# Kernel optimization log

Hardware: AMD Instinct MI355X
Metric: run time of the kernel (lower is better)

The kernel has to match this reference:

```python
import jax, jax.numpy as jnp
import numpy as np

BS, D, C, L_MAP, N_LAYERS, IMG = 8, 512, 128, 8, 9, 64


def _leaky(x):
    return jnp.where(x >= 0, x, 0.2 * x)


def _conv2d_mod(x, style, weight):
    # x: [bs, C, H, W], style: [bs, C], weight: [Cout, Cin, 3, 3]
    # modulate along input-channel dim, demodulate per (sample, out-channel)
    mw = weight[None] * style[:, None, :, None, None]          # [bs, Cout, Cin, 3, 3]
    rstd = jax.lax.rsqrt(jnp.sum(mw * mw, axis=(2, 3, 4), keepdims=True) + 1e-8)
    dw = mw * rstd                                             # demodulated per-sample weights

    def per_sample(xi, wi):
        return jax.lax.conv_general_dilated(
            xi[None], wi, window_strides=(1, 1), padding='SAME',
            dimension_numbers=('NCHW', 'OIHW', 'NCHW'))[0]

    return jax.vmap(per_sample)(x, dw)                         # [bs, C, H, W]


def _upsample2x(x):
    b, c, h, w = x.shape
    return jax.image.resize(x, (b, c, 2 * h, 2 * w), method='bilinear')


def setup_inputs():
    key = jax.random.key(0)
    ks = jax.random.split(key, 10)
    # kaiming fan_in gain for leaky_relu(a=0) per nn.init in Conv2dMod
    conv_std = float(np.sqrt(2.0 / (C * 9)))
    return {
        'latent_z': jax.random.normal(ks[0], (BS, D), jnp.float32),
        'noise': jax.random.normal(ks[1], (N_LAYERS, BS, IMG * IMG), jnp.float32),
        'map_w': jax.random.normal(ks[2], (L_MAP, D, D), jnp.float32) / np.sqrt(D),
        'map_b': jnp.zeros((L_MAP, D), jnp.float32),
        'A_w': jax.random.normal(ks[3], (N_LAYERS, D, C), jnp.float32) / np.sqrt(D),
        'A_b': jax.random.normal(ks[4], (N_LAYERS, C), jnp.float32) * 0.02 + 1.0,
        'B_w': jax.random.normal(ks[5], (N_LAYERS, C), jnp.float32),
        'B_b': jax.random.normal(ks[6], (N_LAYERS, C), jnp.float32) * 0.02,
        'conv_w': jax.random.normal(ks[7], (N_LAYERS, C, C, 3, 3), jnp.float32) * conv_std,
        'rgb_w': jax.random.normal(ks[8], (3, C, 3, 3), jnp.float32) / np.sqrt(C * 9),
        'rgb_b': jnp.zeros((3,), jnp.float32),
    }


def reference(latent_z, noise, map_w, map_b, A_w, A_b, B_w, B_b, conv_w, rgb_w, rgb_b):
    # ---- Mapping: PixelNorm + n_map_layers FC+LeakyReLU ----
    w = latent_z * jax.lax.rsqrt(jnp.mean(latent_z * latent_z, axis=1, keepdims=True) + 1e-8)
    for i in range(L_MAP):
        w = _leaky(w @ map_w[i] + map_b[i])                    # [bs, D] (same w for every style layer)

    # ---- Synthesis ----
    x = jnp.zeros((BS, C, 4, 4), latent_z.dtype)
    for i in range(N_LAYERS):
        if i % 2 == 1:
            x = _upsample2x(x)
        b, c, h, wd = x.shape
        ns = h * wd
        style = w @ A_w[i] + A_b[i]                            # [bs, C]
        # B: Linear(1, C) on per-pixel noise scalar -> per-channel noise map
        nmap = noise[i][:, :ns, None] * B_w[i][None, None, :] + B_b[i]  # [bs, ns, C]
        nmap = jnp.transpose(nmap, (0, 2, 1)).reshape(b, C, h, wd)
        x = _leaky(_conv2d_mod(x, style, conv_w[i]) + nmap)

    # ---- to RGB ----
    rgb = jax.lax.conv_general_dilated(
        x, rgb_w, window_strides=(1, 1), padding='SAME',
        dimension_numbers=('NCHW', 'OIHW', 'NCHW')) + rgb_b[None, :, None, None]
    return rgb
```

## Files before the change

### kernel.cpp

```cpp
#include <hip/hip_runtime.h>
#include <hip/hip_bf16.h>

#define BS 8
#define D 512
#define CCH 128
#define LMAP 8
#define NLAYERS 9

typedef short short8 __attribute__((ext_vector_type(8)));
typedef short short4v __attribute__((ext_vector_type(4)));
typedef float f32x4 __attribute__((ext_vector_type(4)));

__device__ short g_bufA[(size_t)BS * 4096 * CCH];
__device__ short g_bufB[(size_t)BS * 4096 * CCH];
__device__ float g_w[2][BS * D];
__device__ float g_style_all[NLAYERS * BS * CCH];
__device__ float g_rstd_all[NLAYERS * BS * CCH];
__device__ float g_s2[(size_t)NLAYERS * CCH * CCH];
__device__ short g_wpack[(size_t)NLAYERS * 9 * 4 * 8 * 64 * 8];
__device__ short g_rgbpack[9 * 4 * 64 * 8];

__device__ __forceinline__ float leaky(float v) { return v >= 0.f ? v : 0.2f * v; }
__device__ __forceinline__ short f2b(float f) {
    __hip_bfloat16 h = __float2bfloat16(f);
    return *reinterpret_cast<short*>(&h);
}
__device__ __forceinline__ float b2f(short s) {
    return __uint_as_float(((unsigned int)(unsigned short)s) << 16);
}
__device__ __forceinline__ int swz(int col) { return ((col ^ (col >> 3)) & 7) << 3; }

__device__ __forceinline__ void uptaps(int o, int Win, int& i0, int& i1, float& w0, float& w1)
{
    int m = o >> 1;
    if ((o & 1) == 0) { i0 = m - 1; i1 = m; w0 = 0.25f; w1 = 0.75f; if (i0 < 0) { i0 = 0; w0 = 0.f; w1 = 1.f; } }
    else              { i0 = m; i1 = m + 1; w0 = 0.75f; w1 = 0.25f; if (i1 >= Win) { i1 = Win - 1; w0 = 1.f; w1 = 0.f; } }
}

#define WPN (NLAYERS * 9 * 4 * 8 * 64)
#define RGBN (9 * 4 * 64)
#define S2N (NLAYERS * CCH * CCH)
#define NPREPB ((WPN + RGBN + S2N + 255) / 256)
#define NMAPB (32 * BS)

__global__ __launch_bounds__(256) void prep_map0_kernel(
    const float* __restrict__ z, const float* __restrict__ W0, const float* __restrict__ b0,
    const float* __restrict__ convw, const float* __restrict__ rgbw)
{
    const int bid = blockIdx.x;
    const int tid = threadIdx.x;
    if (bid < NMAPB) {
        const int jt = bid & 31, b = bid >> 5;
        const int jb = jt * 16;
        const int jl = tid & 15, kp = tid >> 4;
        __shared__ float xin[D];
        __shared__ float part[16][16];
        __shared__ float wred[4];
        xin[tid] = z[b * D + tid];
        xin[tid + 256] = z[b * D + tid + 256];
        __syncthreads();
        {
            float p = xin[tid] * xin[tid] + xin[tid + 256] * xin[tid + 256];
#pragma unroll
            for (int off = 32; off > 0; off >>= 1) p += __shfl_down(p, off, 64);
            if ((tid & 63) == 0) wred[tid >> 6] = p;
            __syncthreads();
            float ss = wred[0] + wred[1] + wred[2] + wred[3];
            float r = rsqrtf(ss * (1.f / 512.f) + 1e-8f);
            xin[tid] *= r; xin[tid + 256] *= r;
            __syncthreads();
        }
        const float* Wp = W0 + jb + jl;
        const int k0 = kp * 32;
        float a[16];
#pragma unroll
        for (int j = 0; j < 16; ++j) a[j] = 0.f;
#pragma unroll
        for (int k = k0; k < k0 + 32; k += 16) {
#pragma unroll
            for (int j = 0; j < 16; ++j)
                a[j] += xin[k + j] * Wp[(size_t)(k + j) * D];
        }
        float s16 = 0.f;
#pragma unroll
        for (int j = 0; j < 16; ++j) s16 += a[j];
        part[kp][jl] = s16;
        __syncthreads();
        if (tid < 16) {
            float s = b0[jb + tid];
#pragma unroll
            for (int p = 0; p < 16; ++p) s += part[p][tid];
            g_w[1][b * D + jb + tid] = leaky(s);
        }
        return;
    }
    int idx = (bid - NMAPB) * 256 + tid;
    if (idx < WPN) {
        int lane = idx & 63;
        int cogrp = (idx >> 6) & 7;
        int chunk = (idx >> 9) & 3;
        int t = idx >> 11;
        int layer = t / 9, tap = t - layer * 9;
        int co = cogrp * 16 + (lane & 15);
        int ci0 = chunk * 32 + (lane >> 4) * 8;
        short8 v;
#pragma unroll
        for (int j = 0; j < 8; ++j)
            v[j] = f2b(convw[(((size_t)layer * CCH + co) * CCH + ci0 + j) * 9 + tap]);
        *reinterpret_cast<short8*>(&g_wpack[(size_t)idx * 8]) = v;
    } else if (idx < WPN + RGBN) {
        int u = idx - WPN;
        int lane = u & 63;
        int chunk = (u >> 6) & 3;
        int tap = u >> 8;
        int co = lane & 15;
        int ci0 = chunk * 32 + (lane >> 4) * 8;
        short8 v;
#pragma unroll
        for (int j = 0; j < 8; ++j)
            v[j] = (co < 3) ? f2b(rgbw[((size_t)(co * CCH) + ci0 + j) * 9 + tap]) : (short)0;
        *reinterpret_cast<short8*>(&g_rgbpack[(size_t)u * 8]) = v;
    } else if (idx < WPN + RGBN + S2N) {
        int u = idx - WPN - RGBN;
        const float* wp = convw + (size_t)u * 9;
        float s = 0.f;
#pragma unroll
        for (int t = 0; t < 9; ++t) { float m = wp[t]; s += m * m; }
        g_s2[u] = s;
    }
}

__global__ __launch_bounds__(256) void map_fc_kernel(
    int srcSel, const float* __restrict__ W, const float* __restrict__ bias)
{
    float* wout = g_w[srcSel ^ 1];
    int b = blockIdx.y;
    int jb = blockIdx.x * 16;
    int tid = threadIdx.x;
    int jl = tid & 15, kp = tid >> 4;
    __shared__ float xin[D];
    __shared__ float part[16][16];
    const float* win = g_w[srcSel];
    xin[tid] = win[b * D + tid];
    xin[tid + 256] = win[b * D + tid + 256];
    __syncthreads();
    const float* Wp = W + jb + jl;
    const int k0 = kp * 32;
    float a[16];
#pragma unroll
    for (int j = 0; j < 16; ++j) a[j] = 0.f;
#pragma unroll
    for (int k = k0; k < k0 + 32; k += 16) {
#pragma unroll
        for (int j = 0; j < 16; ++j)
            a[j] += xin[k + j] * Wp[(size_t)(k + j) * D];
    }
    float s16 = 0.f;
#pragma unroll
    for (int j = 0; j < 16; ++j) s16 += a[j];
    part[kp][jl] = s16;
    __syncthreads();
    if (tid < 16) {
        float s = bias[jb + tid];
#pragma unroll
        for (int p = 0; p < 16; ++p) s += part[p][tid];
        wout[b * D + jb + tid] = leaky(s);
    }
}

__global__ __launch_bounds__(256) void style_rstd_kernel(
    const float* __restrict__ Aw, const float* __restrict__ Ab)
{
    int l = blockIdx.x + 1;
    int b = blockIdx.y;
    int tid = threadIdx.x;
    __shared__ float ws_[D];
    __shared__ float part[2][CCH];
    __shared__ float st[CCH];
    ws_[tid] = g_w[0][b * D + tid];
    ws_[tid + 256] = g_w[0][b * D + tid + 256];
    __syncthreads();
    {
        int c = tid & 127, kh = tid >> 7;
        const float* Ap = Aw + (size_t)l * D * CCH + c;
        const int k0 = kh * 256;
        float a0 = 0.f, a1 = 0.f, a2 = 0.f, a3 = 0.f, a4 = 0.f, a5 = 0.f, a6 = 0.f, a7 = 0.f;
        for (int k = k0; k < k0 + 256; k += 8) {
            a0 += ws_[k + 0] * Ap[(size_t)(k + 0) * CCH];
            a1 += ws_[k + 1] * Ap[(size_t)(k + 1) * CCH];
            a2 += ws_[k + 2] * Ap[(size_t)(k + 2) * CCH];
            a3 += ws_[k + 3] * Ap[(size_t)(k + 3) * CCH];
            a4 += ws_[k + 4] * Ap[(size_t)(k + 4) * CCH];
            a5 += ws_[k + 5] * Ap[(size_t)(k + 5) * CCH];
            a6 += ws_[k + 6] * Ap[(size_t)(k + 6) * CCH];
            a7 += ws_[k + 7] * Ap[(size_t)(k + 7) * CCH];
        }
        part[kh][c] = ((a0 + a1) + (a2 + a3)) + ((a4 + a5) + (a6 + a7));
    }
    __syncthreads();
    if (tid < CCH) {
        float s = part[0][tid] + part[1][tid] + Ab[l * CCH + tid];
        st[tid] = s;
        g_style_all[((size_t)l * BS + b) * CCH + tid] = s;
    }
    __syncthreads();
    int colid = tid >> 4, kpart = tid & 15;
#pragma unroll
    for (int co8 = 0; co8 < 8; ++co8) {
        int cout = co8 * 16 + colid;
        const float* sp = g_s2 + ((size_t)l * CCH + cout) * CCH + kpart * 8;
        float s = 0.f;
#pragma unroll
        for (int j = 0; j < 8; ++j) { float sv = st[kpart * 8 + j]; s += sv * sv * sp[j]; }
#pragma unroll
        for (int off = 8; off > 0; off >>= 1) s += __shfl_down(s, off, 16);
        if (kpart == 0) g_rstd_all[((size_t)l * BS + b) * CCH + cout] = rsqrtf(s + 1e-8f);
    }
}

__global__ __launch_bounds__(256) void conv8_pair_kernel(
    const float* __restrict__ noise,
    const float* __restrict__ Bw, const float* __restrict__ Bb)
{
    constexpr int W = 8, SW = 10, ROWS = 10, NS = 64, WIN = 4;
    const int b = blockIdx.x;
    const int tid = threadIdx.x;
    const int lane = tid & 63;
    const int wave = tid >> 6;
    const int wpx = wave & 1;
    const int wco = wave >> 1;

    __shared__ short xs1[ROWS * SW * CCH];
    __shared__ short xs2[ROWS * SW * CCH];
    __shared__ short sm[16 * CCH];
    __shared__ float style2_s[CCH], style3_s[CCH];

    if (tid < CCH) {
        style2_s[tid] = g_style_all[((size_t)2 * BS + b) * CCH + tid];
        style3_s[tid] = g_style_all[((size_t)3 * BS + b) * CCH + tid];
    }
    for (int u = tid; u < 16 * CCH; u += 256) {
        int c = u & 127;
        int pp = u >> 7;
        float v = leaky(noise[b * 4096 + pp] * Bw[c] + Bb[c])
                  * g_style_all[((size_t)1 * BS + b) * CCH + c];
        sm[u] = f2b(v);
    }
    for (int u = tid; u < ROWS * SW * 16; u += 256) {
        int ck = u & 15;
        int cell = u >> 4;
        int col = cell % SW;
        int rr = cell / SW;
        if (rr >= 1 && rr <= 8 && col >= 1 && col <= 8) continue;
        short8 zz = {0, 0, 0, 0, 0, 0, 0, 0};
        *reinterpret_cast<short8*>(&xs2[(((rr * SW + col) * CCH) + ck * 8) ^ swz(col)]) = zz;
    }
    __syncthreads();

    for (int u = tid; u < ROWS * SW * 16; u += 256) {
        int ck = u & 15;
        int rem = u >> 4;
        int col = rem % SW;
        int rr = rem / SW;
        int gy = rr - 1, gx = col - 1;
        short8 v = {0, 0, 0, 0, 0, 0, 0, 0};
        if (gy >= 0 && gy < W && gx >= 0 && gx < W) {
            int y0, y1, x0, x1; float wy0, wy1, wx0, wx1;
            uptaps(gy, WIN, y0, y1, wy0, wy1);
            uptaps(gx, WIN, x0, x1, wx0, wx1);
            short8 a00 = *reinterpret_cast<const short8*>(&sm[((size_t)y0 * WIN + x0) * CCH + ck * 8]);
            short8 a01 = *reinterpret_cast<const short8*>(&sm[((size_t)y0 * WIN + x1) * CCH + ck * 8]);
            short8 a10 = *reinterpret_cast<const short8*>(&sm[((size_t)y1 * WIN + x0) * CCH + ck * 8]);
            short8 a11 = *reinterpret_cast<const short8*>(&sm[((size_t)y1 * WIN + x1) * CCH + ck * 8]);
            float w00 = wy0 * wx0, w01 = wy0 * wx1, w10 = wy1 * wx0, w11 = wy1 * wx1;
#pragma unroll
            for (int j = 0; j < 8; ++j)
                v[j] = f2b(w00 * b2f(a00[j]) + w01 * b2f(a01[j])
                         + w10 * b2f(a10[j]) + w11 * b2f(a11[j]));
        }
        *reinterpret_cast<short8*>(&xs1[(((rr * SW + col) * CCH) + ck * 8) ^ swz(col)]) = v;
    }
    __syncthreads();

    int rL[2], cL[2];
#pragma unroll
    for (int pf = 0; pf < 2; ++pf) {
        int pl = (wpx * 2 + pf) * 16 + (lane & 15);
        cL[pf] = pl & (W - 1);
        rL[pf] = pl >> 3;
    }
    const int grpoff = (lane >> 4) * 8;

    {
        f32x4 acc[2][4] = {};
        const short* wl = g_wpack + ((size_t)1 * 9 * 4 * 8 * 64 + (size_t)(wco * 4) * 64 + lane) * 8;
        short8 wc0 = *reinterpret_cast<const short8*>(wl);
        short8 wc1 = *reinterpret_cast<const short8*>(wl + 512);
        short8 wc2 = *reinterpret_cast<const short8*>(wl + 1024);
        short8 wc3 = *reinterpret_cast<const short8*>(wl + 1536);
#pragma unroll
        for (int k = 0; k < 36; ++k) {
            short8 wn0 = wc0, wn1 = wc1, wn2 = wc2, wn3 = wc3;
            if (k + 1 < 36) {
                const short* wk = wl + (size_t)(k + 1) * 4096;
                wn0 = *reinterpret_cast<const short8*>(wk);
                wn1 = *reinterpret_cast<const short8*>(wk + 512);
                wn2 = *reinterpret_cast<const short8*>(wk + 1024);
                wn3 = *reinterpret_cast<const short8*>(wk + 1536);
            }
            const int tap = k >> 2, ch = k & 3;
            const int ky = tap / 3, kx = tap - ky * 3;
#pragma unroll
            for (int pf = 0; pf < 2; ++pf) {
                int col = cL[pf] + kx;
                int idx = (((rL[pf] + ky) * SW + col) * CCH + (ch << 5) + grpoff) ^ swz(col);
                short8 xf = *reinterpret_cast<const short8*>(&xs1[idx]);
                acc[pf][0] = __builtin_amdgcn_mfma_f32_16x16x32_bf16(wc0, xf, acc[pf][0], 0, 0, 0);
                acc[pf][1] = __builtin_amdgcn_mfma_f32_16x16x32_bf16(wc1, xf, acc[pf][1], 0, 0, 0);
                acc[pf][2] = __builtin_amdgcn_mfma_f32_16x16x32_bf16(wc2, xf, acc[pf][2], 0, 0, 0);
                acc[pf][3] = __builtin_amdgcn_mfma_f32_16x16x32_bf16(wc3, xf, acc[pf][3], 0, 0, 0);
            }
            wc0 = wn0; wc1 = wn1; wc2 = wn2; wc3 = wn3;
        }
        float nz[2];
#pragma unroll
        for (int pf = 0; pf < 2; ++pf)
            nz[pf] = noise[(size_t)BS * 4096 + b * 4096 + (wpx * 2 + pf) * 16 + (lane & 15)];
#pragma unroll
        for (int cf = 0; cf < 4; ++cf) {
            const int coB = (wco * 4 + cf) * 16 + (lane >> 4) * 4;
            float rs[4], bw[4], bb[4], sn[4];
#pragma unroll
            for (int r = 0; r < 4; ++r) {
                rs[r] = g_rstd_all[((size_t)1 * BS + b) * CCH + coB + r];
                bw[r] = Bw[1 * CCH + coB + r];
                bb[r] = Bb[1 * CCH + coB + r];
                sn[r] = style2_s[coB + r];
            }
#pragma unroll
            for (int pf = 0; pf < 2; ++pf) {
                int px = (wpx * 2 + pf) * 16 + (lane & 15);
                int y = px >> 3, x = px & 7;
                short4v o;
#pragma unroll
                for (int r = 0; r < 4; ++r)
                    o[r] = f2b(leaky(acc[pf][cf][r] * rs[r] + nz[pf] * bw[r] + bb[r]) * sn[r]);
                int col = x + 1;
                *reinterpret_cast<short4v*>(&xs2[((((y + 1) * SW + col) * CCH) + coB) ^ swz(col)]) = o;
            }
        }
    }
    __syncthreads();

    {
        f32x4 acc[2][4] = {};
        const short* wl = g_wpack + ((size_t)2 * 9 * 4 * 8 * 64 + (size_t)(wco * 4) * 64 + lane) * 8;
        short8 wc0 = *reinterpret_cast<const short8*>(wl);
        short8 wc1 = *reinterpret_cast<const short8*>(wl + 512);
        short8 wc2 = *reinterpret_cast<const short8*>(wl + 1024);
        short8 wc3 = *reinterpret_cast<const short8*>(wl + 1536);
#pragma unroll
        for (int k = 0; k < 36; ++k) {
            short8 wn0 = wc0, wn1 = wc1, wn2 = wc2, wn3 = wc3;
            if (k + 1 < 36) {
                const short* wk = wl + (size_t)(k + 1) * 4096;
                wn0 = *reinterpret_cast<const short8*>(wk);
                wn1 = *reinterpret_cast<const short8*>(wk + 512);
                wn2 = *reinterpret_cast<const short8*>(wk + 1024);
                wn3 = *reinterpret_cast<const short8*>(wk + 1536);
            }
            const int tap = k >> 2, ch = k & 3;
            const int ky = tap / 3, kx = tap - ky * 3;
#pragma unroll
            for (int pf = 0; pf < 2; ++pf) {
                int col = cL[pf] + kx;
                int idx = (((rL[pf] + ky) * SW + col) * CCH + (ch << 5) + grpoff) ^ swz(col);
                short8 xf = *reinterpret_cast<const short8*>(&xs2[idx]);
                acc[pf][0] = __builtin_amdgcn_mfma_f32_16x16x32_bf16(wc0, xf, acc[pf][0], 0, 0, 0);
                acc[pf][1] = __builtin_amdgcn_mfma_f32_16x16x32_bf16(wc1, xf, acc[pf][1], 0, 0, 0);
                acc[pf][2] = __builtin_amdgcn_mfma_f32_16x16x32_bf16(wc2, xf, acc[pf][2], 0, 0, 0);
                acc[pf][3] = __builtin_amdgcn_mfma_f32_16x16x32_bf16(wc3, xf, acc[pf][3], 0, 0, 0);
            }
            wc0 = wn0; wc1 = wn1; wc2 = wn2; wc3 = wn3;
        }
        float nz[2];
#pragma unroll
        for (int pf = 0; pf < 2; ++pf)
            nz[pf] = noise[(size_t)2 * BS * 4096 + b * 4096 + (wpx * 2 + pf) * 16 + (lane & 15)];
#pragma unroll
        for (int cf = 0; cf < 4; ++cf) {
            const int coB = (wco * 4 + cf) * 16 + (lane >> 4) * 4;
            float rs[4], bw[4], bb[4], sn[4];
#pragma unroll
            for (int r = 0; r < 4; ++r) {
                rs[r] = g_rstd_all[((size_t)2 * BS + b) * CCH + coB + r];
                bw[r] = Bw[2 * CCH + coB + r];
                bb[r] = Bb[2 * CCH + coB + r];
                sn[r] = style3_s[coB + r];
            }
#pragma unroll
            for (int pf = 0; pf < 2; ++pf) {
                int px = (wpx * 2 + pf) * 16 + (lane & 15);
                short4v o;
#pragma unroll
                for (int r = 0; r < 4; ++r)
                    o[r] = f2b(leaky(acc[pf][cf][r] * rs[r] + nz[pf] * bw[r] + bb[r]) * sn[r]);
                *reinterpret_cast<short4v*>(&g_bufA[((size_t)b * NS + px) * CCH + coB]) = o;
            }
        }
    }
}

template<int LW, int UPM, int TLW>
__global__ __launch_bounds__(256) void conv_mfma_kernel(
    int srcSel, int layer, int layerNext,
    const float* __restrict__ noise,
    const float* __restrict__ Bw, const float* __restrict__ Bb)
{
    constexpr int W = 1 << LW;
    constexpr int TW = 1 << TLW;
    constexpr int TH = 64 >> TLW;
    constexpr int SW = TW + 2;
    constexpr int ROWS = TH + 2;
    constexpr int NS = W * W;
    constexpr int WIN = W / 2;
    constexpr int TILES_X = W / TW;

    const short* xin = srcSel ? g_bufB : g_bufA;
    short* xout = srcSel ? g_bufA : g_bufB;

    const int b = blockIdx.x & 7;
    const int tileid = blockIdx.x >> 3;
    const int tx = tileid & (TILES_X - 1);
    const int ty = tileid >> (LW - TLW);
    const int rowBase = ty * TH;
    const int colBase = tx * TW;
    const int tid = threadIdx.x;
    const int lane = tid & 63;
    const int wave = tid >> 6;
    const int wpx = wave & 1;
    const int wco = wave >> 1;

    __shared__ short xs[ROWS * SW * CCH];
    __shared__ float style_s[CCH];

    if (tid < CCH)
        style_s[tid] = layerNext ? g_style_all[((size_t)layerNext * BS + b) * CCH + tid] : 1.f;

    {
        const short* src = xin + (size_t)b * NS * CCH;
        const short* srcH = xin + (size_t)b * WIN * WIN * CCH;
        constexpr int UN = ROWS * SW * 16;
        for (int u = tid; u < UN; u += 256) {
            int ck = u & 15;
            int rem = u >> 4;
            int col = rem % SW;
            int rr = rem / SW;
            int gy = rowBase + rr - 1, gx = colBase + col - 1;
            short8 v = {0, 0, 0, 0, 0, 0, 0, 0};
            if (gy >= 0 && gy < W && gx >= 0 && gx < W) {
                if (UPM == 0) {
                    v = *reinterpret_cast<const short8*>(&src[((size_t)gy * W + gx) * CCH + ck * 8]);
                } else {
                    int y0, y1, x0, x1; float wy0, wy1, wx0, wx1;
                    uptaps(gy, WIN, y0, y1, wy0, wy1);
                    uptaps(gx, WIN, x0, x1, wx0, wx1);
                    short8 a00 = *reinterpret_cast<const short8*>(&srcH[((size_t)y0 * WIN + x0) * CCH + ck * 8]);
                    short8 a01 = *reinterpret_cast<const short8*>(&srcH[((size_t)y0 * WIN + x1) * CCH + ck * 8]);
                    short8 a10 = *reinterpret_cast<const short8*>(&srcH[((size_t)y1 * WIN + x0) * CCH + ck * 8]);
                    short8 a11 = *reinterpret_cast<const short8*>(&srcH[((size_t)y1 * WIN + x1) * CCH + ck * 8]);
                    float w00 = wy0 * wx0, w01 = wy0 * wx1, w10 = wy1 * wx0, w11 = wy1 * wx1;
#pragma unroll
                    for (int j = 0; j < 8; ++j)
                        v[j] = f2b(w00 * b2f(a00[j]) + w01 * b2f(a01[j])
                                 + w10 * b2f(a10[j]) + w11 * b2f(a11[j]));
                }
            }
            *reinterpret_cast<short8*>(&xs[(((rr * SW + col) * CCH) + ck * 8) ^ swz(col)]) = v;
        }
    }
    __syncthreads();

    int rL[2], cL[2];
#pragma unroll
    for (int pf = 0; pf < 2; ++pf) {
        int pl = (wpx * 2 + pf) * 16 + (lane & 15);
        cL[pf] = pl & (TW - 1);
        rL[pf] = pl >> TLW;
    }
    const int grpoff = (lane >> 4) * 8;

    f32x4 acc[2][4] = {};
    const short* wl = g_wpack + ((size_t)layer * 9 * 4 * 8 * 64
                                 + (size_t)(wco * 4) * 64 + lane) * 8;

    short8 wc0 = *reinterpret_cast<const short8*>(wl);
    short8 wc1 = *reinterpret_cast<const short8*>(wl + 512);
    short8 wc2 = *reinterpret_cast<const short8*>(wl + 1024);
    short8 wc3 = *reinterpret_cast<const short8*>(wl + 1536);
#pragma unroll
    for (int k = 0; k < 36; ++k) {
        short8 wn0 = wc0, wn1 = wc1, wn2 = wc2, wn3 = wc3;
        if (k + 1 < 36) {
            const short* wk = wl + (size_t)(k + 1) * 4096;
            wn0 = *reinterpret_cast<const short8*>(wk);
            wn1 = *reinterpret_cast<const short8*>(wk + 512);
            wn2 = *reinterpret_cast<const short8*>(wk + 1024);
            wn3 = *reinterpret_cast<const short8*>(wk + 1536);
        }
        const int tap = k >> 2, ch = k & 3;
        const int ky = tap / 3, kx = tap - ky * 3;
#pragma unroll
        for (int pf = 0; pf < 2; ++pf) {
            int col = cL[pf] + kx;
            int idx = (((rL[pf] + ky) * SW + col) * CCH + (ch << 5) + grpoff) ^ swz(col);
            short8 xf = *reinterpret_cast<const short8*>(&xs[idx]);
            acc[pf][0] = __builtin_amdgcn_mfma_f32_16x16x32_bf16(wc0, xf, acc[pf][0], 0, 0, 0);
            acc[pf][1] = __builtin_amdgcn_mfma_f32_16x16x32_bf16(wc1, xf, acc[pf][1], 0, 0, 0);
            acc[pf][2] = __builtin_amdgcn_mfma_f32_16x16x32_bf16(wc2, xf, acc[pf][2], 0, 0, 0);
            acc[pf][3] = __builtin_amdgcn_mfma_f32_16x16x32_bf16(wc3, xf, acc[pf][3], 0, 0, 0);
        }
        wc0 = wn0; wc1 = wn1; wc2 = wn2; wc3 = wn3;
    }

    float nz[2];
    int pxg[2];
#pragma unroll
    for (int pf = 0; pf < 2; ++pf) {
        int pl = (wpx * 2 + pf) * 16 + (lane & 15);
        int x = pl & (TW - 1), y = pl >> TLW;
        pxg[pf] = (rowBase + y) * W + colBase + x;
        nz[pf] = noise[b * 4096 + pxg[pf]];
    }
#pragma unroll
    for (int cf = 0; cf < 4; ++cf) {
        const int coB = (wco * 4 + cf) * 16 + (lane >> 4) * 4;
        float rs[4], bw[4], bb[4], sn[4];
#pragma unroll
        for (int r = 0; r < 4; ++r) {
            rs[r] = g_rstd_all[((size_t)layer * BS + b) * CCH + coB + r];
            bw[r] = Bw[coB + r];
            bb[r] = Bb[coB + r];
            sn[r] = style_s[coB + r];
        }
#pragma unroll
        for (int pf = 0; pf < 2; ++pf) {
            short4v o;
#pragma unroll
            for (int r = 0; r < 4; ++r) {
                float v = leaky(acc[pf][cf][r] * rs[r] + nz[pf] * bw[r] + bb[r]) * sn[r];
                o[r] = f2b(v);
            }
            *reinterpret_cast<short4v*>(&xout[((size_t)b * NS + pxg[pf]) * CCH + coB]) = o;
        }
    }
}

__global__ __launch_bounds__(256) void rgb_mfma_kernel(
    int srcSel, const float* __restrict__ rgbb, float* __restrict__ out)
{
    constexpr int W = 64, TW = 32, TH = 2, SW = 34, ROWS = 4, NS = 4096;
    const short* xin = srcSel ? g_bufB : g_bufA;

    const int b = blockIdx.x & 7;
    const int tileid = blockIdx.x >> 3;
    const int tx = tileid & 1;
    const int ty = tileid >> 1;
    const int rowBase = ty * TH;
    const int colBase = tx * TW;
    const int tid = threadIdx.x;
    const int lane = tid & 63;
    const int wave = tid >> 6;

    __shared__ short xs[ROWS * SW * CCH];

    {
        const short* src = xin + (size_t)b * NS * CCH;
        constexpr int UN = ROWS * SW * 16;
        for (int u = tid; u < UN; u += 256) {
            int ck = u & 15;
            int rem = u >> 4;
            int col = rem % SW;
            int rr = rem / SW;
            int gy = rowBase + rr - 1, gx = colBase + col - 1;
            short8 v = {0, 0, 0, 0, 0, 0, 0, 0};
            if (gy >= 0 && gy < W && gx >= 0 && gx < W)
                v = *reinterpret_cast<const short8*>(&src[((size_t)gy * W + gx) * CCH + ck * 8]);
            *reinterpret_cast<short8*>(&xs[(((rr * SW + col) * CCH) + ck * 8) ^ swz(col)]) = v;
        }
    }
    __syncthreads();

    const int grpoff = (lane >> 4) * 8;
    const int cl = lane & 15;
    f32x4 acc[4] = {};
#pragma unroll
    for (int tap = 0; tap < 9; ++tap) {
        const int ky = tap / 3, kx = tap - ky * 3;
        short8 wf = *reinterpret_cast<const short8*>(
            &g_rgbpack[((size_t)(tap * 4 + wave) * 64 + lane) * 8]);
#pragma unroll
        for (int pf = 0; pf < 4; ++pf) {
            int pl = pf * 16 + cl;
            int x = pl & (TW - 1), y = pl >> 5;
            int col = x + kx;
            int idx = (((y + ky) * SW + col) * CCH + (wave << 5) + grpoff) ^ swz(col);
            short8 xf = *reinterpret_cast<const short8*>(&xs[idx]);
            acc[pf] = __builtin_amdgcn_mfma_f32_16x16x32_bf16(wf, xf, acc[pf], 0, 0, 0);
        }
    }
    __syncthreads();
    float* red = reinterpret_cast<float*>(xs);
    if (wave > 0) {
#pragma unroll
        for (int pf = 0; pf < 4; ++pf)
#pragma unroll
            for (int r = 0; r < 4; ++r)
                red[(((wave - 1) * 4 + pf) * 64 + lane) * 4 + r] = acc[pf][r];
    }
    __syncthreads();
    if (wave == 0 && (lane >> 4) == 0) {
#pragma unroll
        for (int pf = 0; pf < 4; ++pf) {
            int pl = pf * 16 + cl;
            int x = pl & (TW - 1), y = pl >> 5;
            int px = (rowBase + y) * W + colBase + x;
#pragma unroll
            for (int r = 0; r < 3; ++r) {
                float s = acc[pf][r];
#pragma unroll
                for (int wv = 0; wv < 3; ++wv)
                    s += red[((wv * 4 + pf) * 64 + lane) * 4 + r];
                out[(size_t)(b * 3 + r) * NS + px] = s + rgbb[r];
            }
        }
    }
}

extern "C" void kernel_launch(void* const* d_in, const int* in_sizes, int n_in,
                              void* d_out, int out_size, void* d_ws, size_t ws_size,
                              hipStream_t stream)
{
    const float* latent = (const float*)d_in[0];
    const float* noise  = (const float*)d_in[1];
    const float* map_w  = (const float*)d_in[2];
    const float* map_b  = (const float*)d_in[3];
    const float* A_w    = (const float*)d_in[4];
    const float* A_b    = (const float*)d_in[5];
    const float* B_w    = (const float*)d_in[6];
    const float* B_b    = (const float*)d_in[7];
    const float* conv_w = (const float*)d_in[8];
    const float* rgb_w  = (const float*)d_in[9];
    const float* rgb_b  = (const float*)d_in[10];
    float* out = (float*)d_out;
    (void)d_ws; (void)ws_size;

    prep_map0_kernel<<<NMAPB + NPREPB, 256, 0, stream>>>(latent, map_w, map_b, conv_w, rgb_w);

    int wsel = 1;
    for (int i = 1; i < LMAP; ++i) {
        map_fc_kernel<<<dim3(32, BS), 256, 0, stream>>>(
            wsel, map_w + (size_t)i * D * D, map_b + i * D);
        wsel ^= 1;
    }

    style_rstd_kernel<<<dim3(8, BS), 256, 0, stream>>>(A_w, A_b);

    conv8_pair_kernel<<<BS, 256, 0, stream>>>(noise, B_w, B_b);

    int cur = 0;
    int Hc = 8;
    for (int i = 3; i < NLAYERS; ++i) {
        if (i & 1) Hc *= 2;
        int ns = Hc * Hc;
        int lnext = (i < 8) ? (i + 1) : 0;
        int nblk = (ns / 64) * BS;
        const float* nz = noise + (size_t)i * BS * 4096;
        switch (i) {
            case 3: conv_mfma_kernel<4, 1, 4><<<nblk, 256, 0, stream>>>(cur, i, lnext, nz, B_w + i * CCH, B_b + i * CCH); break;
            case 4: conv_mfma_kernel<4, 0, 4><<<nblk, 256, 0, stream>>>(cur, i, lnext, nz, B_w + i * CCH, B_b + i * CCH); break;
            case 5: conv_mfma_kernel<5, 1, 5><<<nblk, 256, 0, stream>>>(cur, i, lnext, nz, B_w + i * CCH, B_b + i * CCH); break;
            case 6: conv_mfma_kernel<5, 0, 5><<<nblk, 256, 0, stream>>>(cur, i, lnext, nz, B_w + i * CCH, B_b + i * CCH); break;
            case 7: conv_mfma_kernel<6, 1, 5><<<nblk, 256, 0, stream>>>(cur, i, lnext, nz, B_w + i * CCH, B_b + i * CCH); break;
            case 8: conv_mfma_kernel<6, 0, 5><<<nblk, 256, 0, stream>>>(cur, i, lnext, nz, B_w + i * CCH, B_b + i * CCH); break;
        }
        cur ^= 1;
    }

    rgb_mfma_kernel<<<64 * BS, 256, 0, stream>>>(cur, rgb_b, out);
}
```

Before: 190.1 us.

## Fuse 16x16 conv layers 3 and 4 into one per-sample kernel

Adds a conv16_pair_kernel that upsamples the 8x8 activation into shared memory, runs layer 3's modulated conv, writes its result back into the same shared tile, then runs layer 4, all in one block per sample. This replaces two conv_mfma_kernel launches and the global round trip of the intermediate activation. In exchange, only BS=8 blocks run, so most CUs sit idle during these layers, and each wave does a long serial MFMA loop. The main loop now starts at layer 5 and switches buffer indices, which must line up with what the fused kernel writes.

New measurement: 234.8 us. +23.5%, slower.

```diff
diff --git a/kernel.cpp b/kernel.cpp
--- a/kernel.cpp
+++ b/kernel.cpp
@@ -401,6 +401,184 @@
 #pragma unroll
             for (int pf = 0; pf < 2; ++pf) {
                 int px = (wpx * 2 + pf) * 16 + (lane & 15);
+                short4v o;
+#pragma unroll
+                for (int r = 0; r < 4; ++r)
+                    o[r] = f2b(leaky(acc[pf][cf][r] * rs[r] + nz[pf] * bw[r] + bb[r]) * sn[r]);
+                *reinterpret_cast<short4v*>(&g_bufA[((size_t)b * NS + px) * CCH + coB]) = o;
+            }
+        }
+    }
+}
+
+__global__ __launch_bounds__(256) void conv16_pair_kernel(
+    const float* __restrict__ noise,
+    const float* __restrict__ Bw, const float* __restrict__ Bb)
+{
+    constexpr int W = 16, SW = 18, ROWS = 18, NS = 256, WIN = 8;
+    const int b = blockIdx.x;
+    const int tid = threadIdx.x;
+    const int lane = tid & 63;
+    const int wave = tid >> 6;
+    const int wpx = wave & 1;
+    const int wco = wave >> 1;
+
+    __shared__ short xs[ROWS * SW * CCH];
+    __shared__ float style4_s[CCH], style5_s[CCH];
+
+    if (tid < CCH) {
+        style4_s[tid] = g_style_all[((size_t)4 * BS + b) * CCH + tid];
+        style5_s[tid] = g_style_all[((size_t)5 * BS + b) * CCH + tid];
+    }
+
+    {
+        const short* src = g_bufA + (size_t)b * WIN * WIN * CCH;
+        for (int u = tid; u < ROWS * SW * 16; u += 256) {
+            int ck = u & 15;
+            int rem = u >> 4;
+            int col = rem % SW;
+            int rr = rem / SW;
+            int gy = rr - 1, gx = col - 1;
+            short8 v = {0, 0, 0, 0, 0, 0, 0, 0};
+            if (gy >= 0 && gy < W && gx >= 0 && gx < W) {
+                int y0, y1, x0, x1; float wy0, wy1, wx0, wx1;
+                uptaps(gy, WIN, y0, y1, wy0, wy1);
+                uptaps(gx, WIN, x0, x1, wx0, wx1);
+                short8 a00 = *reinterpret_cast<const short8*>(&src[((size_t)y0 * WIN + x0) * CCH + ck * 8]);
+                short8 a01 = *reinterpret_cast<const short8*>(&src[((size_t)y0 * WIN + x1) * CCH + ck * 8]);
+                short8 a10 = *reinterpret_cast<const short8*>(&src[((size_t)y1 * WIN + x0) * CCH + ck * 8]);
+                short8 a11 = *reinterpret_cast<const short8*>(&src[((size_t)y1 * WIN + x1) * CCH + ck * 8]);
+                float w00 = wy0 * wx0, w01 = wy0 * wx1, w10 = wy1 * wx0, w11 = wy1 * wx1;
+#pragma unroll
+                for (int j = 0; j < 8; ++j)
+                    v[j] = f2b(w00 * b2f(a00[j]) + w01 * b2f(a01[j])
+                             + w10 * b2f(a10[j]) + w11 * b2f(a11[j]));
+            }
+            *reinterpret_cast<short8*>(&xs[(((rr * SW + col) * CCH) + ck * 8) ^ swz(col)]) = v;
+        }
+    }
+    __syncthreads();
+
+    int rL[8], cL[8];
+#pragma unroll
+    for (int pf = 0; pf < 8; ++pf) {
+        int pl = wpx * 128 + pf * 16 + (lane & 15);
+        cL[pf] = pl & (W - 1);
+        rL[pf] = pl >> 4;
+    }
+    const int grpoff = (lane >> 4) * 8;
+
+    {
+        f32x4 acc[8][4] = {};
+        const short* wl = g_wpack + ((size_t)3 * 9 * 4 * 8 * 64 + (size_t)(wco * 4) * 64 + lane) * 8;
+        short8 wc0 = *reinterpret_cast<const short8*>(wl);
+        short8 wc1 = *reinterpret_cast<const short8*>(wl + 512);
+        short8 wc2 = *reinterpret_cast<const short8*>(wl + 1024);
+        short8 wc3 = *reinterpret_cast<const short8*>(wl + 1536);
+#pragma unroll
+        for (int k = 0; k < 36; ++k) {
+            short8 wn0 = wc0, wn1 = wc1, wn2 = wc2, wn3 = wc3;
+            if (k + 1 < 36) {
+                const short* wk = wl + (size_t)(k + 1) * 4096;
+                wn0 = *reinterpret_cast<const short8*>(wk);
+                wn1 = *reinterpret_cast<const short8*>(wk + 512);
+                wn2 = *reinterpret_cast<const short8*>(wk + 1024);
+                wn3 = *reinterpret_cast<const short8*>(wk + 1536);
+            }
+            const int tap = k >> 2, ch = k & 3;
+            const int ky = tap / 3, kx = tap - ky * 3;
+#pragma unroll
+            for (int pf = 0; pf < 8; ++pf) {
+                int col = cL[pf] + kx;
+                int idx = (((rL[pf] + ky) * SW + col) * CCH + (ch << 5) + grpoff) ^ swz(col);
+                short8 xf = *reinterpret_cast<const short8*>(&xs[idx]);
+                acc[pf][0] = __builtin_amdgcn_mfma_f32_16x16x32_bf16(wc0, xf, acc[pf][0], 0, 0, 0);
+                acc[pf][1] = __builtin_amdgcn_mfma_f32_16x16x32_bf16(wc1, xf, acc[pf][1], 0, 0, 0);
+                acc[pf][2] = __builtin_amdgcn_mfma_f32_16x16x32_bf16(wc2, xf, acc[pf][2], 0, 0, 0);
+                acc[pf][3] = __builtin_amdgcn_mfma_f32_16x16x32_bf16(wc3, xf, acc[pf][3], 0, 0, 0);
+            }
+            wc0 = wn0; wc1 = wn1; wc2 = wn2; wc3 = wn3;
+        }
+        __syncthreads();
+        float nz[8];
+#pragma unroll
+        for (int pf = 0; pf < 8; ++pf)
+            nz[pf] = noise[(size_t)3 * BS * 4096 + b * 4096 + wpx * 128 + pf * 16 + (lane & 15)];
+#pragma unroll
+        for (int cf = 0; cf < 4; ++cf) {
+            const int coB = (wco * 4 + cf) * 16 + (lane >> 4) * 4;
+            float rs[4], bw[4], bb[4], sn[4];
+#pragma unroll
+            for (int r = 0; r < 4; ++r) {
+                rs[r] = g_rstd_all[((size_t)3 * BS + b) * CCH + coB + r];
+                bw[r] = Bw[3 * CCH + coB + r];
+                bb[r] = Bb[3 * CCH + coB + r];
+                sn[r] = style4_s[coB + r];
+            }
+#pragma unroll
+            for (int pf = 0; pf < 8; ++pf) {
+                int px = wpx * 128 + pf * 16 + (lane & 15);
+                int y = px >> 4, x = px & 15;
+                short4v o;
+#pragma unroll
+                for (int r = 0; r < 4; ++r)
+                    o[r] = f2b(leaky(acc[pf][cf][r] * rs[r] + nz[pf] * bw[r] + bb[r]) * sn[r]);
+                int col = x + 1;
+                *reinterpret_cast<short4v*>(&xs[((((y + 1) * SW + col) * CCH) + coB) ^ swz(col)]) = o;
+            }
+        }
+    }
+    __syncthreads();
+
+    {
+        f32x4 acc[8][4] = {};
+        const short* wl = g_wpack + ((size_t)4 * 9 * 4 * 8 * 64 + (size_t)(wco * 4) * 64 + lane) * 8;
+        short8 wc0 = *reinterpret_cast<const short8*>(wl);
+        short8 wc1 = *reinterpret_cast<const short8*>(wl + 512);
+        short8 wc2 = *reinterpret_cast<const short8*>(wl + 1024);
+        short8 wc3 = *reinterpret_cast<const short8*>(wl + 1536);
+#pragma unroll
+        for (int k = 0; k < 36; ++k) {
+            short8 wn0 = wc0, wn1 = wc1, wn2 = wc2, wn3 = wc3;
+            if (k + 1 < 36) {
+                const short* wk = wl + (size_t)(k + 1) * 4096;
+                wn0 = *reinterpret_cast<const short8*>(wk);
+                wn1 = *reinterpret_cast<const short8*>(wk + 512);
+                wn2 = *reinterpret_cast<const short8*>(wk + 1024);
+                wn3 = *reinterpret_cast<const short8*>(wk + 1536);
+            }
+            const int tap = k >> 2, ch = k & 3;
+            const int ky = tap / 3, kx = tap - ky * 3;
+#pragma unroll
+            for (int pf = 0; pf < 8; ++pf) {
+                int col = cL[pf] + kx;
+                int idx = (((rL[pf] + ky) * SW + col) * CCH + (ch << 5) + grpoff) ^ swz(col);
+                short8 xf = *reinterpret_cast<const short8*>(&xs[idx]);
+                acc[pf][0] = __builtin_amdgcn_mfma_f32_16x16x32_bf16(wc0, xf, acc[pf][0], 0, 0, 0);
+                acc[pf][1] = __builtin_amdgcn_mfma_f32_16x16x32_bf16(wc1, xf, acc[pf][1], 0, 0, 0);
+                acc[pf][2] = __builtin_amdgcn_mfma_f32_16x16x32_bf16(wc2, xf, acc[pf][2], 0, 0, 0);
+                acc[pf][3] = __builtin_amdgcn_mfma_f32_16x16x32_bf16(wc3, xf, acc[pf][3], 0, 0, 0);
+            }
+            wc0 = wn0; wc1 = wn1; wc2 = wn2; wc3 = wn3;
+        }
+        float nz[8];
+#pragma unroll
+        for (int pf = 0; pf < 8; ++pf)
+            nz[pf] = noise[(size_t)4 * BS * 4096 + b * 4096 + wpx * 128 + pf * 16 + (lane & 15)];
+#pragma unroll
+        for (int cf = 0; cf < 4; ++cf) {
+            const int coB = (wco * 4 + cf) * 16 + (lane >> 4) * 4;
+            float rs[4], bw[4], bb[4], sn[4];
+#pragma unroll
+            for (int r = 0; r < 4; ++r) {
+                rs[r] = g_rstd_all[((size_t)4 * BS + b) * CCH + coB + r];
+                bw[r] = Bw[4 * CCH + coB + r];
+                bb[r] = Bb[4 * CCH + coB + r];
+                sn[r] = style5_s[coB + r];
+            }
+#pragma unroll
+            for (int pf = 0; pf < 8; ++pf) {
+                int px = wpx * 128 + pf * 16 + (lane & 15);
                 short4v o;
 #pragma unroll
                 for (int r = 0; r < 4; ++r)
@@ -667,18 +845,17 @@
     style_rstd_kernel<<<dim3(8, BS), 256, 0, stream>>>(A_w, A_b);
 
     conv8_pair_kernel<<<BS, 256, 0, stream>>>(noise, B_w, B_b);
+    conv16_pair_kernel<<<BS, 256, 0, stream>>>(noise, B_w, B_b);
 
     int cur = 0;
-    int Hc = 8;
-    for (int i = 3; i < NLAYERS; ++i) {
+    int Hc = 16;
+    for (int i = 5; i < NLAYERS; ++i) {
         if (i & 1) Hc *= 2;
         int ns = Hc * Hc;
         int lnext = (i < 8) ? (i + 1) : 0;
         int nblk = (ns / 64) * BS;
         const float* nz = noise + (size_t)i * BS * 4096;
         switch (i) {
-            case 3: conv_mfma_kernel<4, 1, 4><<<nblk, 256, 0, stream>>>(cur, i, lnext, nz, B_w + i * CCH, B_b + i * CCH); break;
-            case 4: conv_mfma_kernel<4, 0, 4><<<nblk, 256, 0, stream>>>(cur, i, lnext, nz, B_w + i * CCH, B_b + i * CCH); break;
             case 5: conv_mfma_kernel<5, 1, 5><<<nblk, 256, 0, stream>>>(cur, i, lnext, nz, B_w + i * CCH, B_b + i * CCH); break;
             case 6: conv_mfma_kernel<5, 0, 5><<<nblk, 256, 0, stream>>>(cur, i, lnext, nz, B_w + i * CCH, B_b + i * CCH); break;
             case 7: conv_mfma_kernel<6, 1, 5><<<nblk, 256, 0, stream>>>(cur, i, lnext, nz, B_w + i * CCH, B_b + i * CCH); break;
```
